# Kernel tuning notes

Measured on AMD Instinct MI355X. Metric: run time of the kernel, lower is better.

The kernel has to match this reference:

```python
import jax, jax.numpy as jnp
import numpy as np

RHO = 0.5
MASK = 1.0
FR0 = 4096  # ifft length along fast-time axis
FR1 = 512   # fft length along slow-time (Doppler) axis
WIN = 8     # sliding-window length of the phase-reference accumulator
EPS_DENOM = 1e-6


def setup_inputs() -> dict:
    key = jax.random.key(0)
    k1, k2 = jax.random.split(key)
    x_real = jax.random.normal(k1, (8, 4096, 256), dtype=jnp.float32)
    x_imag = jax.random.normal(k2, (8, 4096, 256), dtype=jnp.float32)
    return {"x_real": x_real, "x_imag": x_imag}


def _phase_com_doppler(inp):
    # inp: [B, N, M_in] complex; ifft along last axis padded/truncated to FR0
    final = jnp.fft.ifft(inp, n=FR0, axis=2)  # [B, N, M]
    B, N, M = final.shape
    out0 = final[:, 0, :]                      # [B, M]
    # reproduces the torch `if k < 7` branch without control flow.
    buf0 = jnp.zeros((WIN, B, M), final.dtype).at[WIN - 1].set(out0)

    def step(carry, f_k1):
        pref, buf = carry
        s = jnp.sum(jnp.conj(pref) * f_k1, axis=-1, keepdims=True)  # [B,1]
        phase = s / jnp.abs(s)
        o = f_k1 * jnp.conj(phase)                                  # [B,M]
        pref = pref + o - buf[0]
        buf = jnp.concatenate([buf[1:], o[None]], axis=0)
        return (pref, buf), o

    seq = jnp.swapaxes(final, 0, 1)[1:]        # [N-1, B, M]
    _, outs = jax.lax.scan(step, (out0, buf0), seq)
    out = jnp.concatenate([out0[None], outs], axis=0)  # [N, B, M]
    out = jnp.swapaxes(out, 0, 1)              # [B, N, M]
    # fft along pulse axis padded to FR1
    return jnp.fft.fft(out, n=FR1, axis=1)     # [B, FR1, M]


def reference(x_real, x_imag):
    x = jax.lax.complex(x_real, x_imag)        # [B, P, Q] complex64
    denom = MASK + RHO
    denom = EPS_DENOM if denom == 0 else denom
    x2 = x * (1.0 / denom)
    out3 = _phase_com_doppler(jnp.swapaxes(x2, -1, -2))  # [B, FR1, FR0]
    out3 = jnp.swapaxes(out3, -1, -2)          # [B, FR0, FR1]
    # cs_data dict -> tuple ('input', 'nnline_input')
    return (x, out3)
```

## Files before the change

### kernel.cpp

```cpp
#include <hip/hip_runtime.h>
#include <math.h>

#define NF 4096
#define NC 256
#define NJ 512
#define CH 128
#define TWO_PI_F 6.28318530717958647692f

__device__ __forceinline__ float2 cmul(float2 a, float2 b) {
    return make_float2(a.x*b.x - a.y*b.y, a.x*b.y + a.y*b.x);
}

__device__ __forceinline__ void dft4i(float2& x0, float2& x1, float2& x2, float2& x3, float sgn) {
    float2 t0 = make_float2(x0.x + x2.x, x0.y + x2.y);
    float2 t1 = make_float2(x0.x - x2.x, x0.y - x2.y);
    float2 t2 = make_float2(x1.x + x3.x, x1.y + x3.y);
    float2 t3 = make_float2(x1.x - x3.x, x1.y - x3.y);
    float2 it3 = make_float2(-sgn * t3.y, sgn * t3.x);
    x0 = make_float2(t0.x + t2.x, t0.y + t2.y);
    x2 = make_float2(t0.x - t2.x, t0.y - t2.y);
    x1 = make_float2(t1.x + it3.x, t1.y + it3.y);
    x3 = make_float2(t1.x - it3.x, t1.y - it3.y);
}

__device__ __forceinline__ void dft16(float2* u, float sgn) {
    dft4i(u[0], u[4], u[8],  u[12], sgn);
    dft4i(u[1], u[5], u[9],  u[13], sgn);
    dft4i(u[2], u[6], u[10], u[14], sgn);
    dft4i(u[3], u[7], u[11], u[15], sgn);
    const float C1 = 0.9238795325112867f, S1 = 0.3826834323650898f, R2 = 0.7071067811865476f;
    u[5]  = cmul(u[5],  make_float2(C1,  sgn * S1));
    u[6]  = cmul(u[6],  make_float2(R2,  sgn * R2));
    u[7]  = cmul(u[7],  make_float2(S1,  sgn * C1));
    u[9]  = cmul(u[9],  make_float2(R2,  sgn * R2));
    u[10] = cmul(u[10], make_float2(0.f, sgn));
    u[11] = cmul(u[11], make_float2(-R2, sgn * R2));
    u[13] = cmul(u[13], make_float2(S1,  sgn * C1));
    u[14] = cmul(u[14], make_float2(-R2, sgn * R2));
    u[15] = cmul(u[15], make_float2(-C1, -sgn * S1));
    dft4i(u[0],  u[1],  u[2],  u[3],  sgn);
    dft4i(u[4],  u[5],  u[6],  u[7],  sgn);
    dft4i(u[8],  u[9],  u[10], u[11], sgn);
    dft4i(u[12], u[13], u[14], u[15], sgn);
}

__device__ __forceinline__ void dft8(const float2* u, float2* v, float sgn) {
    float2 e0 = u[0], e1 = u[2], e2 = u[4], e3 = u[6];
    float2 o0 = u[1], o1 = u[3], o2 = u[5], o3 = u[7];
    dft4i(e0, e1, e2, e3, sgn);
    dft4i(o0, o1, o2, o3, sgn);
    const float R2 = 0.7071067811865476f;
    float2 w1 = make_float2(R2, sgn * R2);
    float2 w2 = make_float2(0.f, sgn);
    float2 w3 = make_float2(-R2, sgn * R2);
    float2 t1 = cmul(o1, w1), t2 = cmul(o2, w2), t3 = cmul(o3, w3);
    v[0] = make_float2(e0.x + o0.x, e0.y + o0.y);
    v[4] = make_float2(e0.x - o0.x, e0.y - o0.y);
    v[1] = make_float2(e1.x + t1.x, e1.y + t1.y);
    v[5] = make_float2(e1.x - t1.x, e1.y - t1.y);
    v[2] = make_float2(e2.x + t2.x, e2.y + t2.y);
    v[6] = make_float2(e2.x - t2.x, e2.y - t2.y);
    v[3] = make_float2(e3.x + t3.x, e3.y + t3.y);
    v[7] = make_float2(e3.x - t3.x, e3.y - t3.y);
}

__global__ __launch_bounds__(256) void transpose_kernel(const float* __restrict__ xr,
                                                        const float* __restrict__ xi,
                                                        float2* __restrict__ fin,
                                                        int b0, int nbm1, int nbshift) {
    __shared__ float ldr[64][65];
    __shared__ float ldi[64][65];
    int wg = blockIdx.x;
    int bl = wg & nbm1;
    int rest = wg >> nbshift;
    int ft = rest & 63;
    int ct = rest >> 6;
    int f0 = ft << 6, c0 = ct << 6;
    int t = threadIdx.x;
    int cl = t & 63;
    int rq = t >> 6;
    const float scale = 1.0f / (4096.0f * 1.5f);
    int bg = b0 + bl;
    const float* xrb = xr + (size_t)bg * NF * NC;
    const float* xib = xi + (size_t)bg * NF * NC;
#pragma unroll
    for (int q = 0; q < 16; q++) {
        int r = q * 4 + rq;
        size_t idx = (size_t)(f0 + r) * NC + c0 + cl;
        ldr[cl][r] = xrb[idx] * scale;
        ldi[cl][r] = xib[idx] * scale;
    }
    __syncthreads();
    int fl = t & 63;
#pragma unroll
    for (int q = 0; q < 16; q++) {
        int cr = q * 4 + rq;
        fin[((size_t)(bl * NC + c0 + cr)) * NF + f0 + fl] =
            make_float2(ldr[cr][fl], ldi[cr][fl]);
    }
}

#define IPAD(a) ((a) + ((a) >> 4))

template<int P>
__device__ __forceinline__ void pass16(float2* S, int t, float sgn) {
    const int k = t & (P - 1);
    float2 u[16];
#pragma unroll
    for (int r = 0; r < 16; r++) u[r] = S[IPAD(t + 256 * r)];
    __syncthreads();
    if (P > 1) {
        float ab = sgn * (TWO_PI_F / (16.0f * (float)P)) * (float)k;
#pragma unroll
        for (int r = 1; r < 16; r++) {
            float sn, cs; __sincosf(ab * (float)r, &sn, &cs);
            u[r] = cmul(u[r], make_float2(cs, sn));
        }
    }
    dft16(u, sgn);
    const int base = 16 * P * (t / P) + k;
#pragma unroll
    for (int j = 0; j < 16; j++) {
        const int sl = ((j & 3) << 2) | (j >> 2);
        S[IPAD(base + j * P)] = u[sl];
    }
    __syncthreads();
}

__global__ __launch_bounds__(256) void ifft4096_kernel(float2* __restrict__ fin,
                                                       int bmask, int bshift) {
    __shared__ float2 S[4352];
    int wg = blockIdx.x;
    int bl = wg & bmask;
    int c = wg >> bshift;
    int t = threadIdx.x;
    size_t base = ((size_t)(bl * NC + c)) * NF;
#pragma unroll
    for (int q = 0; q < 16; q++) {
        int f = t + 256 * q;
        S[IPAD(f)] = fin[base + f];
    }
    __syncthreads();
    pass16<1>(S, t, 1.0f);
    pass16<16>(S, t, 1.0f);
    pass16<256>(S, t, 1.0f);
#pragma unroll
    for (int q = 0; q < 16; q++) {
        int f = t + 256 * q;
        fin[base + f] = S[IPAD(f)];
    }
}

#define GSTR 129
__global__ __launch_bounds__(256) void gram_kernel(const float2* __restrict__ fin,
                                                   float2* __restrict__ gpart) {
    __shared__ float lre[40 * GSTR];
    __shared__ float lim[40 * GSTR];
    int wg = blockIdx.x;
    int bl = wg >> 8;
    int ks = (wg >> 5) & 7;
    int ch = wg & 31;
    int m0 = ch * CH;
    int k0 = ks * 32;
    int t = threadIdx.x;
#pragma unroll
    for (int q = 0; q < 20; q++) {
        int e = t + 256 * q;
        int row = e >> 7;
        int m = e & 127;
        int gk = k0 - 8 + row;
        float2 v = (gk >= 0) ? fin[((size_t)(bl * NC + gk)) * NF + m0 + m]
                             : make_float2(0.f, 0.f);
        lre[row * GSTR + m] = v.x;
        lim[row * GSTR + m] = v.y;
    }
    __syncthreads();
    int dgrp = t >> 5;
    int lane = t & 31;
    int d = dgrp + 1;
#pragma unroll
    for (int kk = 0; kk < 32; kk++) {
        int k = k0 + kk;
        float2 acc = make_float2(0.f, 0.f);
        if (k - d >= 0) {
            const float* ar = &lre[(kk + 8 - d) * GSTR];
            const float* ai = &lim[(kk + 8 - d) * GSTR];
            const float* br = &lre[(kk + 8) * GSTR];
            const float* bi = &lim[(kk + 8) * GSTR];
#pragma unroll
            for (int i = 0; i < 4; i++) {
                int m = lane + 32 * i;
                float ax = ar[m], ay = ai[m];
                float bx = br[m], by = bi[m];
                acc.x += ax * bx + ay * by;
                acc.y += ax * by - ay * bx;
            }
        }
#pragma unroll
        for (int off = 16; off >= 1; off >>= 1) {
            acc.x += __shfl_xor(acc.x, off);
            acc.y += __shfl_xor(acc.y, off);
        }
        if (lane == 0)
            gpart[((size_t)(bl * 32 + ch) * NC + k) * 8 + dgrp] = acc;
    }
}

__global__ void gsum_kernel(const float2* __restrict__ gpart, float2* __restrict__ gs, int total) {
    int e = blockIdx.x * blockDim.x + threadIdx.x;
    if (e >= total) return;
    int bl = e >> 11;
    int kd = e & 2047;
    float2 s = make_float2(0.f, 0.f);
    for (int ch = 0; ch < 32; ch++) {
        float2 v = gpart[((size_t)(bl * 32 + ch)) * 2048 + kd];
        s.x += v.x; s.y += v.y;
    }
    gs[e] = s;
}

#define SCAN_STEP(A0, A1, A2, A3, KIDX)  do {                                  \
    float rx0 = p1.x*A0.x - p1.y*A0.y, ry0 = p1.x*A0.y + p1.y*A0.x;            \
    float rx1 = p2.x*A0.z - p2.y*A0.w, ry1 = p2.x*A0.w + p2.y*A0.z;            \
    float rx2 = p3.x*A1.x - p3.y*A1.y, ry2 = p3.x*A1.y + p3.y*A1.x;            \
    float rx3 = p4.x*A1.z - p4.y*A1.w, ry3 = p4.x*A1.w + p4.y*A1.z;            \
    float rx4 = p5.x*A2.x - p5.y*A2.y, ry4 = p5.x*A2.y + p5.y*A2.x;            \
    float rx5 = p6.x*A2.z - p6.y*A2.w, ry5 = p6.x*A2.w + p6.y*A2.z;            \
    float rx6 = p7.x*A3.x - p7.y*A3.y, ry6 = p7.x*A3.y + p7.y*A3.x;            \
    float rx7 = p8.x*A3.z - p8.y*A3.w, ry7 = p8.x*A3.w + p8.y*A3.z;            \
    float sx = ((rx0 + rx1) + (rx2 + rx3)) + ((rx4 + rx5) + (rx6 + rx7));      \
    float sy = ((ry0 + ry1) + (ry2 + ry3)) + ((ry4 + ry5) + (ry6 + ry7));      \
    float inv = rsqrtf(sx * sx + sy * sy);                                     \
    float2 np = make_float2(sx * inv, sy * inv);                               \
    phase[t * NC + (KIDX)] = np;                                               \
    p8 = p7; p7 = p6; p6 = p5; p5 = p4; p4 = p3; p3 = p2; p2 = p1; p1 = np;    \
} while (0)

#define SCAN_LOADG4(BUF, KBASE)  do {                                          \
    _Pragma("unroll") for (int j = 0; j < 4; j++) {                            \
        _Pragma("unroll") for (int q = 0; q < 4; q++)                          \
            BUF[j][q] = gb4[((KBASE) + j) * 4 + q];                            \
    }                                                                          \
} while (0)

#define SCAN_GRP4(BUF, KBASE, FIRST)  do {                                     \
    _Pragma("unroll") for (int j = 0; j < 4; j++) {                            \
        if (FIRST && j == 0) {                                                 \
            phase[t * NC] = make_float2(1.f, 0.f);                             \
        } else {                                                               \
            SCAN_STEP(BUF[j][0], BUF[j][1], BUF[j][2], BUF[j][3], (KBASE) + j);\
        }                                                                      \
    }                                                                          \
} while (0)

__global__ __launch_bounds__(64, 1) void scan_copy_kernel(const float2* __restrict__ gs,
                                                          float2* __restrict__ phase, int nb,
                                                          const float4* __restrict__ csrc,
                                                          float4* __restrict__ cdst, int cn4) {
    if (blockIdx.x != 0) {
        int i = (blockIdx.x - 1) * 64 + threadIdx.x;
        int stride = (gridDim.x - 1) * 64;
        for (; i < cn4; i += stride) cdst[i] = csrc[i];
        return;
    }
    int t = threadIdx.x;
    if (t >= nb) return;
    const float4* gb4 = (const float4*)(gs + (size_t)t * 2048);
    float2 z = make_float2(0.f, 0.f);
    float2 p1 = make_float2(1.f, 0.f);
    float2 p2 = z, p3 = z, p4 = z, p5 = z, p6 = z, p7 = z, p8 = z;
    float4 GA[4][4], GB[4][4];
    SCAN_LOADG4(GA, 0);
    for (int g2 = 0; g2 < 32; g2++) {
        int k0 = g2 * 8;
        SCAN_LOADG4(GB, k0 + 4);
        __builtin_amdgcn_sched_barrier(0);
        if (g2 == 0) { SCAN_GRP4(GA, k0, true); } else { SCAN_GRP4(GA, k0, false); }
        if (g2 < 31) SCAN_LOADG4(GA, k0 + 8);
        __builtin_amdgcn_sched_barrier(0);
        SCAN_GRP4(GB, k0 + 4, false);
    }
}

__global__ void scale_kernel(float4* __restrict__ fin4, const float2* __restrict__ phase, int n4) {
    int i = blockIdx.x * blockDim.x + threadIdx.x;
    if (i >= n4) return;
    int row = i >> 11;
    float2 ph = phase[row];
    float4 v = fin4[i];
    fin4[i] = make_float4(v.x*ph.x + v.y*ph.y, v.y*ph.x - v.x*ph.y,
                          v.z*ph.x + v.w*ph.y, v.w*ph.x - v.z*ph.y);
}

#define FPAD 516

template<int P, bool ZTOP>
__device__ __forceinline__ void pass8x(float2* L, int fp, int i2, float sgn) {
    const int ia = i2, ib = i2 + 32;
    const int ka = ia & (P - 1), kb = ib & (P - 1);
    float2 ua[8], ub[8];
#pragma unroll
    for (int r = 0; r < 8; r++) {
        if (ZTOP && r >= 4) {
            ua[r] = make_float2(0.f, 0.f);
            ub[r] = make_float2(0.f, 0.f);
        } else {
            ua[r] = L[fp * FPAD + ia + 64 * r];
            ub[r] = L[fp * FPAD + ib + 64 * r];
        }
    }
    __syncthreads();
    if (P > 1) {
        float aba = sgn * (TWO_PI_F / (8.0f * (float)P)) * (float)ka;
        float abb = sgn * (TWO_PI_F / (8.0f * (float)P)) * (float)kb;
#pragma unroll
        for (int r = 1; r < 8; r++) {
            float sn, cs;
            __sincosf(aba * (float)r, &sn, &cs);
            ua[r] = cmul(ua[r], make_float2(cs, sn));
            __sincosf(abb * (float)r, &sn, &cs);
            ub[r] = cmul(ub[r], make_float2(cs, sn));
        }
    }
    float2 va[8], vb[8];
    dft8(ua, va, sgn);
    dft8(ub, vb, sgn);
    const int basea = 8 * P * (ia / P) + ka;
    const int baseb = 8 * P * (ib / P) + kb;
#pragma unroll
    for (int r = 0; r < 8; r++) {
        L[fp * FPAD + basea + r * P] = va[r];
        L[fp * FPAD + baseb + r * P] = vb[r];
    }
    __syncthreads();
}

__global__ __launch_bounds__(256) void fft512_kernel(const float2* __restrict__ fin,
                                                     const float2* __restrict__ ph,
                                                     float* __restrict__ outr,
                                                     float2* __restrict__ outc,
                                                     int b0, int realOnly) {
    __shared__ float2 L[8 * FPAD];
    int wg = blockIdx.x;
    int bl = wg >> 9;
    int f0 = (wg & 511) * 8;
    int t = threadIdx.x;
    int fpp = t & 7;
    int cg = t >> 3;
#pragma unroll
    for (int it = 0; it < 8; it++) {
        int c = it * 32 + cg;
        float2 v = fin[((size_t)(bl * NC + c)) * NF + f0 + fpp];
        if (ph) {
            float2 p = ph[bl * NC + c];
            v = make_float2(v.x * p.x + v.y * p.y, v.y * p.x - v.x * p.y);
        }
        L[fpp * FPAD + c] = v;
    }
    __syncthreads();
    int fp = t & 7;
    int i2 = t >> 3;
    pass8x<1, true >(L, fp, i2, -1.0f);
    pass8x<8, false>(L, fp, i2, -1.0f);
    pass8x<64, false>(L, fp, i2, -1.0f);
    size_t ob = ((size_t)((b0 + bl) * NF + f0)) * NJ;
    if (realOnly) {
#pragma unroll
        for (int fp2 = 0; fp2 < 8; fp2++)
#pragma unroll
            for (int jq = 0; jq < 2; jq++) {
                int j = t + 256 * jq;
                outr[ob + (size_t)fp2 * NJ + j] = L[fp2 * FPAD + j].x;
            }
    } else {
#pragma unroll
        for (int fp2 = 0; fp2 < 8; fp2++)
#pragma unroll
            for (int jq = 0; jq < 2; jq++) {
                int j = t + 256 * jq;
                outc[ob + (size_t)fp2 * NJ + j] = L[fp2 * FPAD + j];
            }
    }
}

__global__ void copy_kernel(const float4* __restrict__ src, float4* __restrict__ dst, int n4) {
    int i = blockIdx.x * blockDim.x + threadIdx.x;
    int stride = gridDim.x * blockDim.x;
    for (; i < n4; i += stride) dst[i] = src[i];
}
__global__ void pack_x_kernel(const float2* __restrict__ xr, const float2* __restrict__ xi,
                              float4* __restrict__ out, int n4) {
    int i = blockIdx.x * blockDim.x + threadIdx.x;
    int stride = gridDim.x * blockDim.x;
    for (; i < n4; i += stride) {
        float2 r = xr[i], m = xi[i];
        out[i] = make_float4(r.x, m.x, r.y, m.y);
    }
}

extern "C" void kernel_launch(void* const* d_in, const int* in_sizes, int n_in,
                              void* d_out, int out_size, void* d_ws, size_t ws_size,
                              hipStream_t stream) {
    const float* xr = (const float*)d_in[0];
    const float* xi = (const float*)d_in[1];
    float* out = (float*)d_out;

    if (out_size < 40000000) {
        float* out0r = out;
        float* out3r = out + 8388608;
        size_t need = (size_t)(8388608 + 524288 + 16384 + 2048) * sizeof(float2);
        if (ws_size >= need) {
            float2* fin   = (float2*)d_ws;
            float2* gpart = fin + 8388608;
            float2* gsb   = gpart + 524288;
            float2* phase = gsb + 16384;
            transpose_kernel<<<8 * 256, 256, 0, stream>>>(xr, xi, fin, 0, 7, 3);
            ifft4096_kernel<<<8 * NC, 256, 0, stream>>>(fin, 7, 3);
            gram_kernel<<<8 * 256, 256, 0, stream>>>(fin, gpart);
            gsum_kernel<<<(8 * 2048) / 256, 256, 0, stream>>>(gpart, gsb, 8 * 2048);
            scan_copy_kernel<<<2049, 64, 0, stream>>>(gsb, phase, 8,
                                                      (const float4*)xr, (float4*)out0r, 2097152);
            fft512_kernel<<<8 * 512, 256, 0, stream>>>(fin, phase, out3r, nullptr, 0, 1);
        } else {
            float2* fin   = (float2*)out0r;
            float2* o3f2  = (float2*)out3r;
            float2* gpart = o3f2 + (8388608 - 262144 - 8192 - 1024);
            float2* gsb   = o3f2 + (8388608 - 8192 - 1024);
            float2* phase = o3f2 + (8388608 - 1024);
            for (int p = 0; p < 2; p++) {
                int b0 = p * 4;
                transpose_kernel<<<4 * 256, 256, 0, stream>>>(xr, xi, fin, b0, 3, 2);
                ifft4096_kernel<<<4 * NC, 256, 0, stream>>>(fin, 3, 2);
                gram_kernel<<<4 * 256, 256, 0, stream>>>(fin, gpart);
                gsum_kernel<<<(4 * 2048) / 256, 256, 0, stream>>>(gpart, gsb, 4 * 2048);
                scan_copy_kernel<<<1, 64, 0, stream>>>(gsb, phase, 4, nullptr, nullptr, 0);
                scale_kernel<<<4 * 2048, 256, 0, stream>>>((float4*)fin, phase, 4 * 524288);
                fft512_kernel<<<4 * 512, 256, 0, stream>>>(fin, nullptr, out3r, nullptr, b0, 1);
            }
            copy_kernel<<<2048, 256, 0, stream>>>((const float4*)xr, (float4*)out0r, 2097152);
        }
    } else {
        float2* out0f2 = (float2*)out;
        float2* out3f2 = (float2*)(out + 16777216);
        float2* fin   = out0f2;
        float2* gpart = out3f2 + (16777216 - 524288 - 16384 - 2048);
        float2* gsb   = out3f2 + (16777216 - 16384 - 2048);
        float2* phase = out3f2 + (16777216 - 2048);
        transpose_kernel<<<8 * 256, 256, 0, stream>>>(xr, xi, fin, 0, 7, 3);
        ifft4096_kernel<<<8 * NC, 256, 0, stream>>>(fin, 7, 3);
        gram_kernel<<<8 * 256, 256, 0, stream>>>(fin, gpart);
        gsum_kernel<<<(8 * 2048) / 256, 256, 0, stream>>>(gpart, gsb, 8 * 2048);
        scan_copy_kernel<<<1, 64, 0, stream>>>(gsb, phase, 8, nullptr, nullptr, 0);
        scale_kernel<<<8 * 2048, 256, 0, stream>>>((float4*)fin, phase, 8 * 524288);
        fft512_kernel<<<8 * 512, 256, 0, stream>>>(fin, nullptr, nullptr, out3f2, 0, 0);
        pack_x_kernel<<<4096, 256, 0, stream>>>((const float2*)xr, (const float2*)xi,
                                                (float4*)out0f2, 4194304);
    }
}
```

Before: 186.7 us.

## Restructure gram kernel: per-thread row with all lags, double accumulation

Reassigns gram_kernel work so each thread owns one row k and a stride-8 subset of columns, computing all eight lag products at once. Each B value loaded from LDS is then reused across the eight lags, and the shuffle reduction shrinks to a 3-step tree over 8 lanes. The LDS stride changes from 129 to 136 to suit the new access pattern. Accumulation moves to double precision, which adds FP64 FMAs and conversions and doubles the accumulator register count. The k-d>=0 guard is removed, relying on the zero-filled halo rows.

```diff
diff --git a/kernel.cpp b/kernel.cpp
--- a/kernel.cpp
+++ b/kernel.cpp
@@ -151,7 +151,7 @@
     }
 }
 
-#define GSTR 129
+#define GSTR 136
 __global__ __launch_bounds__(256) void gram_kernel(const float2* __restrict__ fin,
                                                    float2* __restrict__ gpart) {
     __shared__ float lre[40 * GSTR];
@@ -175,34 +175,40 @@
         lim[row * GSTR + m] = v.y;
     }
     __syncthreads();
-    int dgrp = t >> 5;
-    int lane = t & 31;
-    int d = dgrp + 1;
-#pragma unroll
-    for (int kk = 0; kk < 32; kk++) {
-        int k = k0 + kk;
-        float2 acc = make_float2(0.f, 0.f);
-        if (k - d >= 0) {
-            const float* ar = &lre[(kk + 8 - d) * GSTR];
-            const float* ai = &lim[(kk + 8 - d) * GSTR];
-            const float* br = &lre[(kk + 8) * GSTR];
-            const float* bi = &lim[(kk + 8) * GSTR];
-#pragma unroll
-            for (int i = 0; i < 4; i++) {
-                int m = lane + 32 * i;
-                float ax = ar[m], ay = ai[m];
-                float bx = br[m], by = bi[m];
-                acc.x += ax * bx + ay * by;
-                acc.y += ax * by - ay * bx;
-            }
-        }
-#pragma unroll
-        for (int off = 16; off >= 1; off >>= 1) {
-            acc.x += __shfl_xor(acc.x, off);
-            acc.y += __shfl_xor(acc.y, off);
-        }
-        if (lane == 0)
-            gpart[((size_t)(bl * 32 + ch) * NC + k) * 8 + dgrp] = acc;
+    int kk = t >> 3;
+    int sg = t & 7;
+    double accx[8], accy[8];
+#pragma unroll
+    for (int d = 0; d < 8; d++) { accx[d] = 0.0; accy[d] = 0.0; }
+    const float* bre = &lre[(kk + 8) * GSTR + sg];
+    const float* bim = &lim[(kk + 8) * GSTR + sg];
+    const float* are = &lre[kk * GSTR + sg];
+    const float* aim = &lim[kk * GSTR + sg];
+#pragma unroll
+    for (int mm = 0; mm < 16; mm++) {
+        int mo = 8 * mm;
+        double bx = (double)bre[mo];
+        double by = (double)bim[mo];
+#pragma unroll
+        for (int d = 1; d <= 8; d++) {
+            int ao = (8 - d) * GSTR + mo;
+            double ax = (double)are[ao];
+            double ay = (double)aim[ao];
+            accx[d - 1] = fma(ay, by, fma(ax, bx, accx[d - 1]));
+            accy[d - 1] = fma(ax, by, fma(-ay, bx, accy[d - 1]));
+        }
+    }
+    size_t gbase = ((size_t)(bl * 32 + ch) * NC + (k0 + kk)) * 8;
+#pragma unroll
+    for (int d = 0; d < 8; d++) {
+        double sx = accx[d], sy = accy[d];
+#pragma unroll
+        for (int off = 1; off <= 4; off <<= 1) {
+            sx += __shfl_xor(sx, off);
+            sy += __shfl_xor(sy, off);
+        }
+        if (sg == 0)
+            gpart[gbase + d] = make_float2((float)sx, (float)sy);
     }
 }
 
```

After: 180.8 us. 3.2% less time.
